# Performance work log

Measured on AMD Instinct MI355X. Metric: run time of the kernel, lower is better.

Reference implementation:

```python
import jax, jax.numpy as jnp
import numpy as np

B, T, D, K = 64, 1024, 256, 1024
DECAY = 0.99      # ema_decay
BETA = 0.25       # commitment_cost
EPS = 1e-5


def setup_inputs() -> dict:
    key = jax.random.key(0)
    k1, k2 = jax.random.split(key, 2)
    z = jax.random.normal(k1, (B, T, D), dtype=jnp.float32)
    # nn.init.uniform_(embedding.weight, -1/K, 1/K)
    embed = jax.random.uniform(k2, (K, D), dtype=jnp.float32,
                               minval=-1.0 / K, maxval=1.0 / K)
    ema_count = jnp.zeros((K,), dtype=jnp.float32)
    ema_weight = embed  # buffer initialized as a clone of the weight
    return {"z": z, "embed": embed, "ema_count": ema_count, "ema_weight": ema_weight}


def reference(z, embed, ema_count, ema_weight):
    Bq, Tq, Dq = z.shape
    zf = z.reshape(-1, Dq)  # [N, D], N = B*T
    # squared euclidean distances: [N, K]
    dist = (zf * zf).sum(axis=1, keepdims=True) \
        - 2.0 * (zf @ embed.T) \
        + (embed * embed).sum(axis=1)
    idx = jnp.argmin(dist, axis=1)                      # [N]
    q = embed[idx].reshape(Bq, Tq, Dq)                  # nearest codebook vectors

    commit = jnp.mean((z - jax.lax.stop_gradient(q)) ** 2)
    codebook = jnp.mean((q - jax.lax.stop_gradient(z)) ** 2)
    vq_loss = codebook + BETA * commit

    # straight-through estimator
    q_st = z + jax.lax.stop_gradient(q - z)

    # EMA codebook update (training-mode, no_grad in torch)
    counts = jax.ops.segment_sum(jnp.ones((zf.shape[0],), zf.dtype), idx, num_segments=K)
    dw = jax.ops.segment_sum(zf, idx, num_segments=K)   # one_hot.T @ z_flat, [K, D]
    new_count = DECAY * ema_count + (1.0 - DECAY) * counts
    new_ema_w = DECAY * ema_weight + (1.0 - DECAY) * dw
    n = new_count.sum()
    cs = (new_count + EPS) / (n + K * EPS) * n          # laplace-smoothed counts
    new_embed = new_ema_w / cs[:, None]

    return (q_st, vq_loss, idx.reshape(Bq, Tq), new_embed, new_count, new_ema_w)
```

## Files before the change

kernel.cpp:

```cpp
#include <hip/hip_runtime.h>
#include <cfloat>

#define N_Q     65536
#define D_DIM   256
#define K_CODES 1024
#define DELTA   0.004f
#define MARGIN  0.001f
#define SW_CAP  1536
#define SPILL_CAP 65536

#define OUT_QST   0
#define OUT_LOSS  16777216
#define OUT_IDX   16777217
#define OUT_EMBED 16842753
#define OUT_COUNT 17104897
#define OUT_EMAW  17105921

#define WS_IDX    0u
#define WS_ZZ     262144u
#define WS_PERM   524288u
#define WS_PACK   786432u
#define WS_EN     1310720u
#define WS_ICNT   1314816u
#define WS_OFFS   1318912u
#define WS_OFFW   1323008u
#define WS_CNTF   1327104u
#define WS_CS     1331200u
#define WS_ET     1335296u
#define WS_LOSSB  1859584u
#define WS_SPCNT  1867776u

typedef short          bf16x8 __attribute__((ext_vector_type(8)));
typedef unsigned short u16x8  __attribute__((ext_vector_type(8)));
typedef float          f32x4  __attribute__((ext_vector_type(4)));

__device__ inline unsigned short f2bf(float x) {
    unsigned u = __float_as_uint(x);
    u += 0x7FFFu + ((u >> 16) & 1u);
    return (unsigned short)(u >> 16);
}
__device__ inline float bf2f(unsigned short h) {
    return __uint_as_float((unsigned)h << 16);
}
__device__ inline u16x8 pack8(float4 a, float4 b) {
    u16x8 p;
    p[0]=f2bf(a.x); p[1]=f2bf(a.y); p[2]=f2bf(a.z); p[3]=f2bf(a.w);
    p[4]=f2bf(b.x); p[5]=f2bf(b.y); p[6]=f2bf(b.z); p[7]=f2bf(b.w);
    return p;
}
__device__ inline void gll16(const void* g, void* l) {
    __builtin_amdgcn_global_load_lds(
        (const __attribute__((address_space(1))) unsigned int*)g,
        (__attribute__((address_space(3))) unsigned int*)l, 16, 0, 0);
}
#define SWZMIN(x, PAT) fminf((x), __int_as_float( \
    __builtin_amdgcn_ds_swizzle(__float_as_int(x), (PAT))))

__global__ void prep_kernel(const float* __restrict__ embed,
                            unsigned short* __restrict__ et,
                            unsigned long long* __restrict__ pack,
                            float* __restrict__ enorm,
                            int* __restrict__ icnt,
                            double* __restrict__ lossb,
                            int* __restrict__ spc)
{
    int b = blockIdx.x, t = threadIdx.x;
    if (b < 128) {
        int tid = b * 256 + t;
        int k16 = tid >> 9, d8 = (tid >> 4) & 31, col = tid & 15;
        const float* src = &embed[(size_t)(k16 * 16 + col) * D_DIM + d8 * 8];
        float4 a = *(const float4*)&src[0];
        float4 c = *(const float4*)&src[4];
        *(u16x8*)&et[(size_t)tid * 8] = pack8(a, c);
        unsigned long long* p = pack + (size_t)tid * 2;
        p[0] = ~0ull; p[1] = ~0ull;
    } else {
        int b2 = b - 128;
        int wave = t >> 6, lane = t & 63;
        int rbase = (b2 * 4 + wave) * 8;
        for (int i = 0; i < 8; ++i) {
            int r = rbase + i;
            const float4 v = *(const float4*)&embed[(size_t)r * D_DIM + lane * 4];
            float s = v.x * v.x + v.y * v.y + v.z * v.z + v.w * v.w;
            #pragma unroll
            for (int m = 32; m >= 1; m >>= 1) s += __shfl_down(s, m, 64);
            if (lane == 0) enorm[r] = s;
        }
        if (b2 == 0) {
            #pragma unroll
            for (int i = 0; i < 4; ++i) {
                icnt[t * 4 + i] = 0;
                lossb[t * 4 + i] = 0.0;
            }
            if (t == 0) *spc = 0;
        }
    }
}

__launch_bounds__(512, 4)
__global__ void sweep_kernel(const float* __restrict__ z,
                             const float* __restrict__ embed,
                             const unsigned short* __restrict__ et,
                             const float* __restrict__ enorm,
                             float* __restrict__ zzg,
                             unsigned long long* __restrict__ pack,
                             unsigned* __restrict__ spill,
                             int* __restrict__ spc)
{
    __shared__ unsigned short Eb[2][16384];
    __shared__ unsigned list[SW_CAP];
    __shared__ unsigned short s1h[SW_CAP];
    __shared__ float Ens[K_CODES];
    __shared__ float rminS[128];
    __shared__ float zzS[128];
    __shared__ int lcnt;

    const int t = threadIdx.x;
    const int w = t >> 6, lane = t & 63;
    const int col = lane & 15, quad = lane >> 4;
    const int qbase = blockIdx.x * 128;

    if (t == 0) lcnt = 0;
    for (int i = t; i < K_CODES; i += 512) Ens[i] = enorm[i];

    {
        const unsigned short* src = et + w * 2048 + lane * 8;
        unsigned short* dst = &Eb[0][w * 2048];
        #pragma unroll
        for (int i = 0; i < 4; ++i) gll16(src + i * 512, dst + i * 512);
    }

    bf16x8 A[8];
    {
        float s = 0.f;
        #pragma unroll
        for (int ds = 0; ds < 8; ++ds) {
            const float* zp = &z[(size_t)(qbase + w*16 + col) * D_DIM
                                 + ds*32 + quad*8];
            float4 a = *(const float4*)zp;
            float4 b = *(const float4*)(zp + 4);
            s += a.x*a.x + a.y*a.y + a.z*a.z + a.w*a.w
               + b.x*b.x + b.y*b.y + b.z*b.z + b.w*b.w;
            u16x8 p = pack8(a, b);
            A[ds] = *(bf16x8*)&p;
        }
        s += __shfl_xor(s, 16, 64);
        s += __shfl_xor(s, 32, 64);
        if (quad == 0) {
            zzg[qbase + w*16 + col] = s;
            zzS[w*16 + col] = s;
        }
    }

    float rmin[4];
    #pragma unroll
    for (int i = 0; i < 4; ++i) rmin[i] = FLT_MAX;

    asm volatile("s_waitcnt vmcnt(0) lgkmcnt(0)" ::: "memory");
    __builtin_amdgcn_s_barrier();
    __builtin_amdgcn_sched_barrier(0);

    #pragma unroll 1
    for (int kc = 0; kc < 16; ++kc) {
        if (kc < 15) {
            const unsigned short* src = et + (kc + 1) * 16384 + w * 2048 + lane * 8;
            unsigned short* dst = &Eb[(kc + 1) & 1][w * 2048];
            #pragma unroll
            for (int i = 0; i < 4; ++i) gll16(src + i * 512, dst + i * 512);
        }

        const unsigned short* buf = Eb[kc & 1];
        f32x4 acc[4];
        #pragma unroll
        for (int ct = 0; ct < 4; ++ct)
            acc[ct] = (f32x4){0.f, 0.f, 0.f, 0.f};

        #pragma unroll
        for (int ds = 0; ds < 8; ++ds) {
            bf16x8 B[4];
            #pragma unroll
            for (int ct = 0; ct < 4; ++ct)
                B[ct] = *(const bf16x8*)&buf[((ct*32 + ds*4 + quad)*16 + col)*8];
            #pragma unroll
            for (int ct = 0; ct < 4; ++ct)
                acc[ct] = __builtin_amdgcn_mfma_f32_16x16x32_bf16(A[ds], B[ct], acc[ct], 0, 0, 0);
        }

        float en4[4];
        #pragma unroll
        for (int ct = 0; ct < 4; ++ct) en4[ct] = Ens[kc*64 + ct*16 + col];

        float s1v[4][4];
        #pragma unroll
        for (int ct = 0; ct < 4; ++ct)
            #pragma unroll
            for (int rg = 0; rg < 4; ++rg)
                s1v[ct][rg] = fmaf(-2.0f, acc[ct][rg], en4[ct]);

        float m4[4];
        #pragma unroll
        for (int rg = 0; rg < 4; ++rg)
            m4[rg] = fminf(fminf(s1v[0][rg], s1v[1][rg]),
                           fminf(s1v[2][rg], s1v[3][rg]));

        #pragma unroll
        for (int i = 0; i < 4; ++i) m4[i] = SWZMIN(m4[i], 0x041F);
        #pragma unroll
        for (int i = 0; i < 4; ++i) m4[i] = SWZMIN(m4[i], 0x081F);
        #pragma unroll
        for (int i = 0; i < 4; ++i) m4[i] = SWZMIN(m4[i], 0x101F);
        #pragma unroll
        for (int i = 0; i < 4; ++i) m4[i] = SWZMIN(m4[i], 0x201F);

        float thrv[4];
        #pragma unroll
        for (int i = 0; i < 4; ++i) {
            rmin[i] = fminf(rmin[i], m4[i]);
            thrv[i] = rmin[i] + DELTA;
        }

        #pragma unroll
        for (int rg = 0; rg < 4; ++rg) {
            float th = thrv[rg];
            #pragma unroll
            for (int ct = 0; ct < 4; ++ct) {
                if (s1v[ct][rg] <= th) {
                    int k    = kc*64 + ct*16 + col;
                    int qloc = w*16 + quad*4 + rg;
                    int pos  = atomicAdd(&lcnt, 1);
                    if (pos < SW_CAP) {
                        list[pos] = ((unsigned)qloc << 10) | (unsigned)k;
                        s1h[pos]  = f2bf(s1v[ct][rg]);
                    } else {
                        int sp = atomicAdd(spc, 1);
                        if (sp < SPILL_CAP) {
                            spill[sp] = ((unsigned)(qbase + qloc) << 10)
                                      | (unsigned)k;
                            asm volatile("s_waitcnt vmcnt(0)" ::: "memory");
                        }
                    }
                }
            }
        }

        asm volatile("s_waitcnt vmcnt(4)" ::: "memory");
        __builtin_amdgcn_s_barrier();
        __builtin_amdgcn_sched_barrier(0);
    }

    if (col == 0) {
        #pragma unroll
        for (int rg = 0; rg < 4; ++rg)
            rminS[w*16 + quad*4 + rg] = rmin[rg];
    }
    asm volatile("s_waitcnt lgkmcnt(0)" ::: "memory");
    __builtin_amdgcn_s_barrier();
    __builtin_amdgcn_sched_barrier(0);
    asm volatile("" ::: "memory");

    int cnt = lcnt; if (cnt > SW_CAP) cnt = SW_CAP;
    int gid = t >> 3, gl = t & 7;
    for (int e = gid; e < cnt; e += 64) {
        unsigned ent = list[e];
        int qloc = (int)(ent >> 10), k = (int)(ent & 1023u);
        if (bf2f(s1h[e]) > rminS[qloc] + (DELTA + MARGIN)) continue;
        int qg = qbase + qloc;
        const float* zp  = &z[(size_t)qg * D_DIM + gl * 32];
        const float* epf = &embed[(size_t)k * D_DIM + gl * 32];
        double d0 = 0.0, d1 = 0.0;
        #pragma unroll
        for (int i = 0; i < 4; ++i) {
            float4 a  = *(const float4*)&zp[i*8];
            float4 b  = *(const float4*)&epf[i*8];
            float4 c  = *(const float4*)&zp[i*8 + 4];
            float4 dv = *(const float4*)&epf[i*8 + 4];
            d0 += (double)a.x*b.x + (double)a.y*b.y + (double)a.z*b.z + (double)a.w*b.w;
            d1 += (double)c.x*dv.x + (double)c.y*dv.y + (double)c.z*dv.z + (double)c.w*dv.w;
        }
        double dd = d0 + d1;
        #pragma unroll
        for (int m = 1; m < 8; m <<= 1) dd += __shfl_xor(dd, m, 64);
        if (gl == 0) {
            float s = (zzS[qloc] - 2.0f*(float)dd) + Ens[k];
            unsigned long long pk =
                ((unsigned long long)__float_as_uint(s) << 32) | (unsigned)k;
            atomicMin(&pack[qg], pk);
        }
    }
}

__global__ void spill_kernel(const float* __restrict__ z,
                             const float* __restrict__ embed,
                             const float* __restrict__ enorm,
                             const float* __restrict__ zz,
                             const unsigned* __restrict__ spill,
                             const int* __restrict__ spc,
                             unsigned long long* __restrict__ pack)
{
    int cnt = *spc; if (cnt > SPILL_CAP) cnt = SPILL_CAP;
    int gid = (blockIdx.x * 256 + threadIdx.x) >> 3, gl = threadIdx.x & 7;
    int stride = (gridDim.x * 256) >> 3;
    for (int e = gid; e < cnt; e += stride) {
        unsigned ent = spill[e];
        int qg = (int)(ent >> 10), k = (int)(ent & 1023u);
        const float* zp  = &z[(size_t)qg * D_DIM + gl * 32];
        const float* epf = &embed[(size_t)k * D_DIM + gl * 32];
        double dd = 0.0;
        #pragma unroll
        for (int i = 0; i < 8; ++i) {
            float4 a = *(const float4*)&zp[i*4];
            float4 b = *(const float4*)&epf[i*4];
            dd += (double)a.x*b.x + (double)a.y*b.y
                + (double)a.z*b.z + (double)a.w*b.w;
        }
        #pragma unroll
        for (int m = 1; m < 8; m <<= 1) dd += __shfl_xor(dd, m, 64);
        if (gl == 0) {
            float s = (zz[qg] - 2.0f*(float)dd) + enorm[k];
            unsigned long long pk =
                ((unsigned long long)__float_as_uint(s) << 32) | (unsigned)k;
            atomicMin(&pack[qg], pk);
        }
    }
}

__global__ void unpack_kernel(const unsigned long long* __restrict__ pack,
                              int* __restrict__ idx_i,
                              float* __restrict__ idx_f,
                              int* __restrict__ icnt)
{
    int n = blockIdx.x * 256 + threadIdx.x;
    int k = (int)(pack[n] & 0xffffffffull);
    idx_i[n] = k;
    idx_f[n] = (float)k;
    atomicAdd(&icnt[k], 1);
}

__global__ void scan_kernel(const int* __restrict__ icnt,
                            int* __restrict__ offs,
                            int* __restrict__ offw,
                            float* __restrict__ cntf)
{
    __shared__ int s[1024];
    int t = threadIdx.x;
    int v0 = icnt[t];
    s[t] = v0;
    __syncthreads();
    for (int d = 1; d < 1024; d <<= 1) {
        int v = (t >= d) ? s[t - d] : 0;
        __syncthreads();
        s[t] += v;
        __syncthreads();
    }
    int excl = s[t] - v0;
    offs[t] = excl;
    offw[t] = excl;
    cntf[t] = (float)v0;
}

__global__ void fill_kernel(const int* __restrict__ idx,
                            int* __restrict__ offw,
                            int* __restrict__ perm)
{
    int n = blockIdx.x * 256 + threadIdx.x;
    int k = idx[n];
    int pos = atomicAdd(&offw[k], 1);
    perm[pos] = n;
}

__global__ void qst_loss_kernel(const float* __restrict__ z,
                                const float* __restrict__ embed,
                                const int* __restrict__ idx,
                                float* __restrict__ qst,
                                double* __restrict__ lossb)
{
    int tid = blockIdx.x * blockDim.x + threadIdx.x;
    int e0  = tid * 4;
    int n   = e0 >> 8, d = e0 & 255;
    int k   = idx[n];
    const float4 q4 = *(const float4*)&embed[(size_t)k * D_DIM + d];
    const float4 z4 = *(const float4*)&z[e0];
    float4 o;
    o.x = z4.x + (q4.x - z4.x);
    o.y = z4.y + (q4.y - z4.y);
    o.z = z4.z + (q4.z - z4.z);
    o.w = z4.w + (q4.w - z4.w);
    *(float4*)&qst[e0] = o;
    float dx = z4.x - q4.x, dy = z4.y - q4.y, dz = z4.z - q4.z, dw = z4.w - q4.w;
    float s = dx * dx + dy * dy + dz * dz + dw * dw;
    #pragma unroll
    for (int m = 32; m >= 1; m >>= 1) s += __shfl_down(s, m, 64);
    __shared__ float ps[4];
    int wave = threadIdx.x >> 6, lane = threadIdx.x & 63;
    if (lane == 0) ps[wave] = s;
    __syncthreads();
    if (threadIdx.x == 0)
        atomicAdd(&lossb[blockIdx.x & 1023],
                  (double)((ps[0] + ps[1]) + (ps[2] + ps[3])));
}

__global__ void fin_counts_kernel(const float* __restrict__ ema_count,
                                  const float* __restrict__ cntf,
                                  const double* __restrict__ lossb,
                                  float* __restrict__ out_count,
                                  float* __restrict__ out_loss,
                                  float* __restrict__ cs)
{
    __shared__ float  red[1024];
    __shared__ double dred[1024];
    int t = threadIdx.x;
    float c = 0.99f * ema_count[t] + 0.01f * cntf[t];
    out_count[t] = c;
    red[t]  = c;
    dred[t] = lossb[t];
    __syncthreads();
    for (int s = 512; s >= 1; s >>= 1) {
        if (t < s) { red[t] += red[t + s]; dred[t] += dred[t + s]; }
        __syncthreads();
    }
    float n = red[0];
    cs[t] = (c + 1e-5f) / (n + 1024.0f * 1e-5f) * n;
    if (t == 0) {
        float m = (float)(dred[0] / (double)((size_t)N_Q * D_DIM));
        out_loss[0] = m + 0.25f * m;
    }
}

__global__ void accum_embed_kernel(const float* __restrict__ z,
                                   const int* __restrict__ perm,
                                   const int* __restrict__ icnt,
                                   const int* __restrict__ offs,
                                   const float* __restrict__ cs,
                                   const float* __restrict__ ema_w,
                                   float* __restrict__ out_embed,
                                   float* __restrict__ out_emaw)
{
    __shared__ int rows[256];
    int k = blockIdx.x, t = threadIdx.x;
    int cnt = icnt[k], off = offs[k];
    double a0 = 0.0, a1 = 0.0, a2 = 0.0, a3 = 0.0;
    for (int base = 0; base < cnt; base += 256) {
        int m = min(256, cnt - base);
        __syncthreads();
        if (t < m) rows[t] = perm[off + base + t];
        __syncthreads();
        int r = 0;
        for (; r + 4 <= m; r += 4) {
            a0 += (double)z[(size_t)rows[r+0] * D_DIM + t];
            a1 += (double)z[(size_t)rows[r+1] * D_DIM + t];
            a2 += (double)z[(size_t)rows[r+2] * D_DIM + t];
            a3 += (double)z[(size_t)rows[r+3] * D_DIM + t];
        }
        for (; r < m; ++r) a0 += (double)z[(size_t)rows[r] * D_DIM + t];
    }
    double acc = (a0 + a1) + (a2 + a3);
    float w = 0.99f * ema_w[(size_t)k * D_DIM + t] + 0.01f * (float)acc;
    out_emaw[(size_t)k * D_DIM + t]  = w;
    out_embed[(size_t)k * D_DIM + t] = w / cs[k];
}

extern "C" void kernel_launch(void* const* d_in, const int* in_sizes, int n_in,
                              void* d_out, int out_size, void* d_ws, size_t ws_size,
                              hipStream_t stream)
{
    const float* z          = (const float*)d_in[0];
    const float* embed      = (const float*)d_in[1];
    const float* ema_count  = (const float*)d_in[2];
    const float* ema_weight = (const float*)d_in[3];
    float* out = (float*)d_out;
    char*  ws  = (char*)d_ws;

    int*      ws_idx  = (int*)(ws + WS_IDX);
    unsigned* ws_spill= (unsigned*)(ws + WS_IDX);
    float*    ws_zz   = (float*)(ws + WS_ZZ);
    int*      ws_perm = (int*)(ws + WS_PERM);
    unsigned long long* ws_pack = (unsigned long long*)(ws + WS_PACK);
    float*    ws_en   = (float*)(ws + WS_EN);
    int*      ws_icnt = (int*)(ws + WS_ICNT);
    int*      ws_offs = (int*)(ws + WS_OFFS);
    int*      ws_offw = (int*)(ws + WS_OFFW);
    float*    ws_cntf = (float*)(ws + WS_CNTF);
    float*    ws_cs   = (float*)(ws + WS_CS);
    unsigned short* ws_et = (unsigned short*)(ws + WS_ET);
    double*   ws_lb   = (double*)(ws + WS_LOSSB);
    int*      ws_spc  = (int*)(ws + WS_SPCNT);

    prep_kernel<<<160, 256, 0, stream>>>(embed, ws_et, ws_pack, ws_en,
                                         ws_icnt, ws_lb, ws_spc);

    sweep_kernel<<<N_Q / 128, 512, 0, stream>>>(z, embed, ws_et, ws_en, ws_zz,
                                                ws_pack, ws_spill, ws_spc);

    spill_kernel<<<32, 256, 0, stream>>>(z, embed, ws_en, ws_zz,
                                         ws_spill, ws_spc, ws_pack);

    unpack_kernel<<<N_Q / 256, 256, 0, stream>>>(ws_pack, ws_idx,
                                                 out + OUT_IDX, ws_icnt);
    scan_kernel<<<1, 1024, 0, stream>>>(ws_icnt, ws_offs, ws_offw, ws_cntf);
    fill_kernel<<<N_Q / 256, 256, 0, stream>>>(ws_idx, ws_offw, ws_perm);
    qst_loss_kernel<<<(N_Q * (D_DIM / 4)) / 256, 256, 0, stream>>>(
        z, embed, ws_idx, out + OUT_QST, ws_lb);
    fin_counts_kernel<<<1, 1024, 0, stream>>>(ema_count, ws_cntf, ws_lb,
                                              out + OUT_COUNT, out + OUT_LOSS, ws_cs);
    accum_embed_kernel<<<K_CODES, 256, 0, stream>>>(z, ws_perm, ws_icnt, ws_offs,
                                                    ws_cs, ema_weight,
                                                    out + OUT_EMBED, out + OUT_EMAW);
}
```

Measured before the change: 284.7 us.

## Split codebook across blocks with two row tiles per wave; fuse unpack into qst

The sweep kernel now gives each block 256 queries against one half of the codebook (512 codes). Each wave holds two 16-row A tiles, so every B fragment loaded from LDS feeds two MFMAs, and the grid still has 512 blocks. The unpack and qst/loss kernels are merged into one kernel that reads the packed argmin once per query and writes idx, counts, the straight-through output and loss partials, dropping a launch and an idx round-trip. The cost is that candidate filtering is now relative to each half's own minimum, which can add refinement candidates and list spills, and the prefetch wait tightens to vmcnt(0).

```diff
diff --git a/kernel.cpp b/kernel.cpp
--- a/kernel.cpp
+++ b/kernel.cpp
@@ -110,70 +110,79 @@
     __shared__ unsigned short Eb[2][16384];
     __shared__ unsigned list[SW_CAP];
     __shared__ unsigned short s1h[SW_CAP];
-    __shared__ float Ens[K_CODES];
-    __shared__ float rminS[128];
-    __shared__ float zzS[128];
+    __shared__ float Ens[512];
+    __shared__ float rminS[256];
+    __shared__ float zzS[256];
     __shared__ int lcnt;
 
     const int t = threadIdx.x;
     const int w = t >> 6, lane = t & 63;
     const int col = lane & 15, quad = lane >> 4;
-    const int qbase = blockIdx.x * 128;
+    const int qb   = blockIdx.x & 255;
+    const int half = blockIdx.x >> 8;
+    const int qbase = qb * 256;
+    const int koff  = half * 512;
+    const unsigned short* etH = et + (size_t)half * (512 * 256);
 
     if (t == 0) lcnt = 0;
-    for (int i = t; i < K_CODES; i += 512) Ens[i] = enorm[i];
+    Ens[t] = enorm[koff + t];
 
     {
-        const unsigned short* src = et + w * 2048 + lane * 8;
+        const unsigned short* src = etH + w * 2048 + lane * 8;
         unsigned short* dst = &Eb[0][w * 2048];
         #pragma unroll
         for (int i = 0; i < 4; ++i) gll16(src + i * 512, dst + i * 512);
     }
 
-    bf16x8 A[8];
-    {
+    bf16x8 A[2][8];
+    #pragma unroll
+    for (int rt = 0; rt < 2; ++rt) {
         float s = 0.f;
         #pragma unroll
         for (int ds = 0; ds < 8; ++ds) {
-            const float* zp = &z[(size_t)(qbase + w*16 + col) * D_DIM
+            const float* zp = &z[(size_t)(qbase + w*32 + rt*16 + col) * D_DIM
                                  + ds*32 + quad*8];
             float4 a = *(const float4*)zp;
             float4 b = *(const float4*)(zp + 4);
             s += a.x*a.x + a.y*a.y + a.z*a.z + a.w*a.w
                + b.x*b.x + b.y*b.y + b.z*b.z + b.w*b.w;
             u16x8 p = pack8(a, b);
-            A[ds] = *(bf16x8*)&p;
+            A[rt][ds] = *(bf16x8*)&p;
         }
         s += __shfl_xor(s, 16, 64);
         s += __shfl_xor(s, 32, 64);
         if (quad == 0) {
-            zzg[qbase + w*16 + col] = s;
-            zzS[w*16 + col] = s;
-        }
-    }
-
-    float rmin[4];
+            if (half == 0) zzg[qbase + w*32 + rt*16 + col] = s;
+            zzS[w*32 + rt*16 + col] = s;
+        }
+    }
+
+    float rmin[2][4];
     #pragma unroll
-    for (int i = 0; i < 4; ++i) rmin[i] = FLT_MAX;
+    for (int rt = 0; rt < 2; ++rt)
+        #pragma unroll
+        for (int rg = 0; rg < 4; ++rg) rmin[rt][rg] = FLT_MAX;
 
     asm volatile("s_waitcnt vmcnt(0) lgkmcnt(0)" ::: "memory");
     __builtin_amdgcn_s_barrier();
     __builtin_amdgcn_sched_barrier(0);
 
     #pragma unroll 1
-    for (int kc = 0; kc < 16; ++kc) {
-        if (kc < 15) {
-            const unsigned short* src = et + (kc + 1) * 16384 + w * 2048 + lane * 8;
+    for (int kc = 0; kc < 8; ++kc) {
+        if (kc < 7) {
+            const unsigned short* src = etH + (kc + 1) * 16384 + w * 2048 + lane * 8;
             unsigned short* dst = &Eb[(kc + 1) & 1][w * 2048];
             #pragma unroll
             for (int i = 0; i < 4; ++i) gll16(src + i * 512, dst + i * 512);
         }
 
         const unsigned short* buf = Eb[kc & 1];
-        f32x4 acc[4];
-        #pragma unroll
-        for (int ct = 0; ct < 4; ++ct)
-            acc[ct] = (f32x4){0.f, 0.f, 0.f, 0.f};
+        f32x4 acc[2][4];
+        #pragma unroll
+        for (int rt = 0; rt < 2; ++rt)
+            #pragma unroll
+            for (int ct = 0; ct < 4; ++ct)
+                acc[rt][ct] = (f32x4){0.f, 0.f, 0.f, 0.f};
 
         #pragma unroll
         for (int ds = 0; ds < 8; ++ds) {
@@ -182,81 +191,85 @@
             for (int ct = 0; ct < 4; ++ct)
                 B[ct] = *(const bf16x8*)&buf[((ct*32 + ds*4 + quad)*16 + col)*8];
             #pragma unroll
+            for (int ct = 0; ct < 4; ++ct) {
+                acc[0][ct] = __builtin_amdgcn_mfma_f32_16x16x32_bf16(A[0][ds], B[ct], acc[0][ct], 0, 0, 0);
+                acc[1][ct] = __builtin_amdgcn_mfma_f32_16x16x32_bf16(A[1][ds], B[ct], acc[1][ct], 0, 0, 0);
+            }
+        }
+
+        #pragma unroll
+        for (int rt = 0; rt < 2; ++rt) {
+            float en4[4];
+            #pragma unroll
+            for (int ct = 0; ct < 4; ++ct) en4[ct] = Ens[kc*64 + ct*16 + col];
+
+            float s1v[4][4];
+            #pragma unroll
             for (int ct = 0; ct < 4; ++ct)
-                acc[ct] = __builtin_amdgcn_mfma_f32_16x16x32_bf16(A[ds], B[ct], acc[ct], 0, 0, 0);
-        }
-
-        float en4[4];
-        #pragma unroll
-        for (int ct = 0; ct < 4; ++ct) en4[ct] = Ens[kc*64 + ct*16 + col];
-
-        float s1v[4][4];
-        #pragma unroll
-        for (int ct = 0; ct < 4; ++ct)
+                #pragma unroll
+                for (int rg = 0; rg < 4; ++rg)
+                    s1v[ct][rg] = fmaf(-2.0f, acc[rt][ct][rg], en4[ct]);
+
+            float m4[4];
             #pragma unroll
             for (int rg = 0; rg < 4; ++rg)
-                s1v[ct][rg] = fmaf(-2.0f, acc[ct][rg], en4[ct]);
-
-        float m4[4];
-        #pragma unroll
-        for (int rg = 0; rg < 4; ++rg)
-            m4[rg] = fminf(fminf(s1v[0][rg], s1v[1][rg]),
-                           fminf(s1v[2][rg], s1v[3][rg]));
-
-        #pragma unroll
-        for (int i = 0; i < 4; ++i) m4[i] = SWZMIN(m4[i], 0x041F);
-        #pragma unroll
-        for (int i = 0; i < 4; ++i) m4[i] = SWZMIN(m4[i], 0x081F);
-        #pragma unroll
-        for (int i = 0; i < 4; ++i) m4[i] = SWZMIN(m4[i], 0x101F);
-        #pragma unroll
-        for (int i = 0; i < 4; ++i) m4[i] = SWZMIN(m4[i], 0x201F);
-
-        float thrv[4];
-        #pragma unroll
-        for (int i = 0; i < 4; ++i) {
-            rmin[i] = fminf(rmin[i], m4[i]);
-            thrv[i] = rmin[i] + DELTA;
-        }
-
-        #pragma unroll
-        for (int rg = 0; rg < 4; ++rg) {
-            float th = thrv[rg];
-            #pragma unroll
-            for (int ct = 0; ct < 4; ++ct) {
-                if (s1v[ct][rg] <= th) {
-                    int k    = kc*64 + ct*16 + col;
-                    int qloc = w*16 + quad*4 + rg;
-                    int pos  = atomicAdd(&lcnt, 1);
-                    if (pos < SW_CAP) {
-                        list[pos] = ((unsigned)qloc << 10) | (unsigned)k;
-                        s1h[pos]  = f2bf(s1v[ct][rg]);
-                    } else {
-                        int sp = atomicAdd(spc, 1);
-                        if (sp < SPILL_CAP) {
-                            spill[sp] = ((unsigned)(qbase + qloc) << 10)
-                                      | (unsigned)k;
-                            asm volatile("s_waitcnt vmcnt(0)" ::: "memory");
+                m4[rg] = fminf(fminf(s1v[0][rg], s1v[1][rg]),
+                               fminf(s1v[2][rg], s1v[3][rg]));
+
+            #pragma unroll
+            for (int i = 0; i < 4; ++i) m4[i] = SWZMIN(m4[i], 0x041F);
+            #pragma unroll
+            for (int i = 0; i < 4; ++i) m4[i] = SWZMIN(m4[i], 0x081F);
+            #pragma unroll
+            for (int i = 0; i < 4; ++i) m4[i] = SWZMIN(m4[i], 0x101F);
+            #pragma unroll
+            for (int i = 0; i < 4; ++i) m4[i] = SWZMIN(m4[i], 0x201F);
+
+            float thrv[4];
+            #pragma unroll
+            for (int i = 0; i < 4; ++i) {
+                rmin[rt][i] = fminf(rmin[rt][i], m4[i]);
+                thrv[i] = rmin[rt][i] + DELTA;
+            }
+
+            #pragma unroll
+            for (int rg = 0; rg < 4; ++rg) {
+                float th = thrv[rg];
+                #pragma unroll
+                for (int ct = 0; ct < 4; ++ct) {
+                    if (s1v[ct][rg] <= th) {
+                        int k    = koff + kc*64 + ct*16 + col;
+                        int qloc = w*32 + rt*16 + quad*4 + rg;
+                        int pos  = atomicAdd(&lcnt, 1);
+                        if (pos < SW_CAP) {
+                            list[pos] = ((unsigned)qloc << 10) | (unsigned)k;
+                            s1h[pos]  = f2bf(s1v[ct][rg]);
+                        } else {
+                            int sp = atomicAdd(spc, 1);
+                            if (sp < SPILL_CAP)
+                                spill[sp] = ((unsigned)(qbase + qloc) << 10)
+                                          | (unsigned)k;
                         }
                     }
                 }
             }
         }
 
-        asm volatile("s_waitcnt vmcnt(4)" ::: "memory");
+        asm volatile("s_waitcnt vmcnt(0)" ::: "memory");
         __builtin_amdgcn_s_barrier();
         __builtin_amdgcn_sched_barrier(0);
     }
 
     if (col == 0) {
         #pragma unroll
-        for (int rg = 0; rg < 4; ++rg)
-            rminS[w*16 + quad*4 + rg] = rmin[rg];
+        for (int rt = 0; rt < 2; ++rt)
+            #pragma unroll
+            for (int rg = 0; rg < 4; ++rg)
+                rminS[w*32 + rt*16 + quad*4 + rg] = rmin[rt][rg];
     }
     asm volatile("s_waitcnt lgkmcnt(0)" ::: "memory");
     __builtin_amdgcn_s_barrier();
     __builtin_amdgcn_sched_barrier(0);
-    asm volatile("" ::: "memory");
 
     int cnt = lcnt; if (cnt > SW_CAP) cnt = SW_CAP;
     int gid = t >> 3, gl = t & 7;
@@ -281,7 +294,7 @@
         #pragma unroll
         for (int m = 1; m < 8; m <<= 1) dd += __shfl_xor(dd, m, 64);
         if (gl == 0) {
-            float s = (zzS[qloc] - 2.0f*(float)dd) + Ens[k];
+            float s = (zzS[qloc] - 2.0f*(float)dd) + Ens[k & 511];
             unsigned long long pk =
                 ((unsigned long long)__float_as_uint(s) << 32) | (unsigned)k;
             atomicMin(&pack[qg], pk);
@@ -324,60 +337,30 @@
     }
 }
 
-__global__ void unpack_kernel(const unsigned long long* __restrict__ pack,
-                              int* __restrict__ idx_i,
-                              float* __restrict__ idx_f,
-                              int* __restrict__ icnt)
-{
-    int n = blockIdx.x * 256 + threadIdx.x;
-    int k = (int)(pack[n] & 0xffffffffull);
-    idx_i[n] = k;
-    idx_f[n] = (float)k;
-    atomicAdd(&icnt[k], 1);
-}
-
-__global__ void scan_kernel(const int* __restrict__ icnt,
-                            int* __restrict__ offs,
-                            int* __restrict__ offw,
-                            float* __restrict__ cntf)
-{
-    __shared__ int s[1024];
-    int t = threadIdx.x;
-    int v0 = icnt[t];
-    s[t] = v0;
+__global__ void qst_unpack_kernel(const unsigned long long* __restrict__ pack,
+                                  const float* __restrict__ z,
+                                  const float* __restrict__ embed,
+                                  int* __restrict__ idx_i,
+                                  float* __restrict__ idx_f,
+                                  int* __restrict__ icnt,
+                                  float* __restrict__ qst,
+                                  double* __restrict__ lossb)
+{
+    __shared__ int ks[4];
+    int b = blockIdx.x, t = threadIdx.x;
+    int n0 = b * 4;
+    if (t < 4) {
+        int k = (int)(pack[n0 + t] & 0xffffffffull);
+        ks[t] = k;
+        idx_i[n0 + t] = k;
+        idx_f[n0 + t] = (float)k;
+        atomicAdd(&icnt[k], 1);
+    }
     __syncthreads();
-    for (int d = 1; d < 1024; d <<= 1) {
-        int v = (t >= d) ? s[t - d] : 0;
-        __syncthreads();
-        s[t] += v;
-        __syncthreads();
-    }
-    int excl = s[t] - v0;
-    offs[t] = excl;
-    offw[t] = excl;
-    cntf[t] = (float)v0;
-}
-
-__global__ void fill_kernel(const int* __restrict__ idx,
-                            int* __restrict__ offw,
-                            int* __restrict__ perm)
-{
-    int n = blockIdx.x * 256 + threadIdx.x;
-    int k = idx[n];
-    int pos = atomicAdd(&offw[k], 1);
-    perm[pos] = n;
-}
-
-__global__ void qst_loss_kernel(const float* __restrict__ z,
-                                const float* __restrict__ embed,
-                                const int* __restrict__ idx,
-                                float* __restrict__ qst,
-                                double* __restrict__ lossb)
-{
-    int tid = blockIdx.x * blockDim.x + threadIdx.x;
-    int e0  = tid * 4;
-    int n   = e0 >> 8, d = e0 & 255;
-    int k   = idx[n];
+    int e0 = b * 1024 + t * 4;
+    int qi = t >> 6;
+    int d  = (t * 4) & 255;
+    int k  = ks[qi];
     const float4 q4 = *(const float4*)&embed[(size_t)k * D_DIM + d];
     const float4 z4 = *(const float4*)&z[e0];
     float4 o;
@@ -391,12 +374,44 @@
     #pragma unroll
     for (int m = 32; m >= 1; m >>= 1) s += __shfl_down(s, m, 64);
     __shared__ float ps[4];
-    int wave = threadIdx.x >> 6, lane = threadIdx.x & 63;
+    int wave = t >> 6, lane = t & 63;
     if (lane == 0) ps[wave] = s;
     __syncthreads();
-    if (threadIdx.x == 0)
-        atomicAdd(&lossb[blockIdx.x & 1023],
+    if (t == 0)
+        atomicAdd(&lossb[b & 1023],
                   (double)((ps[0] + ps[1]) + (ps[2] + ps[3])));
+}
+
+__global__ void scan_kernel(const int* __restrict__ icnt,
+                            int* __restrict__ offs,
+                            int* __restrict__ offw,
+                            float* __restrict__ cntf)
+{
+    __shared__ int s[1024];
+    int t = threadIdx.x;
+    int v0 = icnt[t];
+    s[t] = v0;
+    __syncthreads();
+    for (int d = 1; d < 1024; d <<= 1) {
+        int v = (t >= d) ? s[t - d] : 0;
+        __syncthreads();
+        s[t] += v;
+        __syncthreads();
+    }
+    int excl = s[t] - v0;
+    offs[t] = excl;
+    offw[t] = excl;
+    cntf[t] = (float)v0;
+}
+
+__global__ void fill_kernel(const int* __restrict__ idx,
+                            int* __restrict__ offw,
+                            int* __restrict__ perm)
+{
+    int n = blockIdx.x * 256 + threadIdx.x;
+    int k = idx[n];
+    int pos = atomicAdd(&offw[k], 1);
+    perm[pos] = n;
 }
 
 __global__ void fin_counts_kernel(const float* __restrict__ ema_count,
@@ -488,18 +503,17 @@
     prep_kernel<<<160, 256, 0, stream>>>(embed, ws_et, ws_pack, ws_en,
                                          ws_icnt, ws_lb, ws_spc);
 
-    sweep_kernel<<<N_Q / 128, 512, 0, stream>>>(z, embed, ws_et, ws_en, ws_zz,
-                                                ws_pack, ws_spill, ws_spc);
+    sweep_kernel<<<512, 512, 0, stream>>>(z, embed, ws_et, ws_en, ws_zz,
+                                          ws_pack, ws_spill, ws_spc);
 
     spill_kernel<<<32, 256, 0, stream>>>(z, embed, ws_en, ws_zz,
                                          ws_spill, ws_spc, ws_pack);
 
-    unpack_kernel<<<N_Q / 256, 256, 0, stream>>>(ws_pack, ws_idx,
-                                                 out + OUT_IDX, ws_icnt);
+    qst_unpack_kernel<<<N_Q / 4, 256, 0, stream>>>(ws_pack, z, embed,
+                                                   ws_idx, out + OUT_IDX,
+                                                   ws_icnt, out + OUT_QST, ws_lb);
     scan_kernel<<<1, 1024, 0, stream>>>(ws_icnt, ws_offs, ws_offw, ws_cntf);
     fill_kernel<<<N_Q / 256, 256, 0, stream>>>(ws_idx, ws_offw, ws_perm);
-    qst_loss_kernel<<<(N_Q * (D_DIM / 4)) / 256, 256, 0, stream>>>(
-        z, embed, ws_idx, out + OUT_QST, ws_lb);
     fin_counts_kernel<<<1, 1024, 0, stream>>>(ema_count, ws_cntf, ws_lb,
                                               out + OUT_COUNT, out + OUT_LOSS, ws_cs);
     accum_embed_kernel<<<K_CODES, 256, 0, stream>>>(z, ws_perm, ws_icnt, ws_offs,
```

Result: slower. 357.0 us (+25.4%).
